# Performance work log

Hardware: AMD Instinct MI355X
Metric: run time of the kernel (lower is better)

The kernel has to match this reference:

```python
import jax, jax.numpy as jnp
import numpy as np

B = 8192
I = 1024
H = 1024


def setup_inputs() -> dict:
    key = jax.random.key(0)
    ks = jax.random.split(key, 7)
    s_in = 1.0 / np.sqrt(I)
    s_h = 1.0 / np.sqrt(H)
    return {
        "x_current": jax.random.normal(ks[0], (B, I), dtype=jnp.float32),
        "c_previous": jax.random.normal(ks[1], (B, H), dtype=jnp.float32),
        "h_previous": jax.random.normal(ks[2], (B, H), dtype=jnp.float32),
        # stacked gate weights, order (i, f, o, g); equivalent to 8 small nn.Linear
        "Wx": jax.random.normal(ks[3], (4 * H, I), dtype=jnp.float32) * s_in,
        "bx": jax.random.normal(ks[4], (4 * H,), dtype=jnp.float32) * s_in,
        "Wh": jax.random.normal(ks[5], (4 * H, H), dtype=jnp.float32) * s_h,
        "bh": jax.random.normal(ks[6], (4 * H,), dtype=jnp.float32) * s_h,
    }


def reference(x_current, c_previous, h_previous, Wx, bx, Wh, bh):
    # two fused GEMMs covering all 8 original linears: [B, 4H]
    gates = (jnp.einsum("bi,gi->bg", x_current, Wx) + bx
             + jnp.einsum("bh,gh->bg", h_previous, Wh) + bh)
    i_g, f_g, o_g, g_g = jnp.split(gates, 4, axis=-1)
    input_gate = jax.nn.sigmoid(i_g)
    forget_gate = jax.nn.sigmoid(f_g)
    output_gate = jax.nn.sigmoid(o_g)
    g_current = jnp.tanh(g_g)
    c_current = forget_gate * c_previous + input_gate * g_current
    h_current = output_gate * jnp.tanh(c_current)
    return (c_current, h_current)
```

## Files before the change

### kernel.cpp

```cpp
#include <hip/hip_runtime.h>
#include <hip/hip_bf16.h>

#define Bsz 8192
#define Isz 1024
#define Hsz 1024
#define Ksz 2048
#define Nsz 4096

#define BM 128
#define BN 128
#define BK 64

typedef __attribute__((ext_vector_type(8))) short bf16x8;
typedef __attribute__((ext_vector_type(4))) float f32x4;
typedef __attribute__((ext_vector_type(8))) unsigned short ushort8;

__device__ __forceinline__ void async_copy16(const void* g, void* l) {
  __builtin_amdgcn_global_load_lds(
      (const __attribute__((address_space(1))) void*)g,
      (__attribute__((address_space(3))) void*)l, 16, 0, 0);
}

__device__ __forceinline__ float sigmoid_f(float x) {
  return 1.0f / (1.0f + __expf(-x));
}
__device__ __forceinline__ float tanh_f(float x) {
  x = fminf(15.0f, fmaxf(-15.0f, x));
  const float e = __expf(-2.0f * x);
  return (1.0f - e) / (1.0f + e);
}

__device__ __forceinline__ unsigned short bfc(float f) {
  return __builtin_bit_cast(unsigned short, __float2bfloat16(f));
}
__device__ __forceinline__ ushort8 cvt8v(float4 v0, float4 v1) {
  ushort8 o;
  o[0] = bfc(v0.x); o[1] = bfc(v0.y); o[2] = bfc(v0.z); o[3] = bfc(v0.w);
  o[4] = bfc(v1.x); o[5] = bfc(v1.y); o[6] = bfc(v1.z); o[7] = bfc(v1.w);
  return o;
}

__global__ __launch_bounds__(256) void prep_kernel(
    const float* __restrict__ x, const float* __restrict__ h,
    const float* __restrict__ Wx, const float* __restrict__ Wh,
    const float* __restrict__ bx, const float* __restrict__ bh,
    __hip_bfloat16* __restrict__ Abf, __hip_bfloat16* __restrict__ Wbf,
    float* __restrict__ bsum) {
  const int idx = blockIdx.x * 256 + threadIdx.x;
  const int ATH = (Bsz * Ksz) / 8;
  if (idx < ATH) {
    const int b = idx >> 8;
    const int k = (idx & 255) << 3;
    const float* src = (k < Isz) ? (x + (size_t)b * Isz + k)
                                 : (h + (size_t)b * Hsz + (k - Isz));
    const float4 v0 = ((const float4*)src)[0];
    const float4 v1 = ((const float4*)src)[1];
    *(ushort8*)(Abf + (size_t)b * Ksz + k) = cvt8v(v0, v1);
  } else {
    const int t2 = idx - ATH;
    const int r = t2 >> 8;
    const int k = (t2 & 255) << 3;
    const int hh = r >> 2, g = r & 3;
    const float* src = (k < Isz) ? (Wx + (size_t)(g * Hsz + hh) * Isz + k)
                                 : (Wh + (size_t)(g * Hsz + hh) * Hsz + (k - Isz));
    const float4 v0 = ((const float4*)src)[0];
    const float4 v1 = ((const float4*)src)[1];
    *(ushort8*)(Wbf + (size_t)r * Ksz + k) = cvt8v(v0, v1);
  }
  if (idx < Nsz) {
    const int hh = idx >> 2, g = idx & 3;
    bsum[idx] = bx[g * Hsz + hh] + bh[g * Hsz + hh];
  }
}

__global__ __launch_bounds__(256) void lstm_gemm_kernel(
    const __hip_bfloat16* __restrict__ A,
    const __hip_bfloat16* __restrict__ W,
    const float* __restrict__ bsum,
    const float* __restrict__ c_prev,
    float* __restrict__ c_out,
    float* __restrict__ h_out) {
  __shared__ ulong2 smem_raw[2048];
  __hip_bfloat16* As = (__hip_bfloat16*)smem_raw;
  __hip_bfloat16* Bs = As + BM * BK;

  const int tid = threadIdx.x;
  const int lane = tid & 63;
  const int wave = tid >> 6;
  const int wm = wave & 1;
  const int wn = wave >> 1;
  const int row0 = blockIdx.x * BM;
  const int col0 = blockIdx.y * BN;

  const __hip_bfloat16* Ag = A + (size_t)row0 * Ksz;
  const __hip_bfloat16* Wg = W + (size_t)col0 * Ksz;

  int srow[4], sofs[4];
#pragma unroll
  for (int p = 0; p < 4; p++) {
    const int c = tid + p * 256;
    srow[p] = c >> 3;
    sofs[p] = ((c & 7) ^ ((c >> 3) & 7)) << 3;
  }

  f32x4 acc[4][4] = {};

  const int q = lane >> 4;
  const int cl = lane & 15;
  const int phi = cl & 7;

  for (int kt = 0; kt < Ksz; kt += BK) {
    __syncthreads();
#pragma unroll
    for (int p = 0; p < 4; p++)
      async_copy16(Ag + (size_t)srow[p] * Ksz + kt + sofs[p],
                   (char*)As + (tid + p * 256) * 16);
#pragma unroll
    for (int p = 0; p < 4; p++)
      async_copy16(Wg + (size_t)srow[p] * Ksz + kt + sofs[p],
                   (char*)Bs + (tid + p * 256) * 16);
    __syncthreads();

#pragma unroll
    for (int ks = 0; ks < 2; ks++) {
      const int jsw = ((ks * 4 + q) ^ phi) << 3;
      bf16x8 af[4], bfr[4];
#pragma unroll
      for (int i = 0; i < 4; i++)
        af[i] = *(const bf16x8*)(As + (wm * 64 + i * 16 + cl) * BK + jsw);
#pragma unroll
      for (int j = 0; j < 4; j++)
        bfr[j] = *(const bf16x8*)(Bs + (wn * 64 + j * 16 + cl) * BK + jsw);
#pragma unroll
      for (int i = 0; i < 4; i++)
#pragma unroll
        for (int j = 0; j < 4; j++)
          acc[i][j] = __builtin_amdgcn_mfma_f32_16x16x32_bf16(
              af[i], bfr[j], acc[i][j], 0, 0, 0);
    }
  }

  __syncthreads();
  float* E = (float*)smem_raw + wave * (16 * 68);

  float bj[4];
#pragma unroll
  for (int j = 0; j < 4; j++)
    bj[j] = bsum[col0 + wn * 64 + j * 16 + cl];

  const int hw = (col0 >> 2) + wn * 16;
  const int r16 = lane >> 2;
  const int tt = lane & 3;

#pragma unroll
  for (int i = 0; i < 4; i++) {
#pragma unroll
    for (int j = 0; j < 4; j++)
#pragma unroll
      for (int r = 0; r < 4; r++)
        E[(q * 4 + r) * 68 + j * 16 + cl] = acc[i][j][r] + bj[j];
    __builtin_amdgcn_wave_barrier();
    const float* Er = E + r16 * 68 + tt * 16;
    const float4 f0 = ((const float4*)Er)[0];
    const float4 f1 = ((const float4*)Er)[1];
    const float4 f2 = ((const float4*)Er)[2];
    const float4 f3 = ((const float4*)Er)[3];

    const int row = row0 + wm * 64 + i * 16 + r16;
    const size_t off = (size_t)row * Hsz + hw + tt * 4;
    const float4 cp4 = *(const float4*)(c_prev + off);
    float4 c4, h4;
    {
      const float cn = sigmoid_f(f0.y) * cp4.x + sigmoid_f(f0.x) * tanh_f(f0.w);
      c4.x = cn; h4.x = sigmoid_f(f0.z) * tanh_f(cn);
    }
    {
      const float cn = sigmoid_f(f1.y) * cp4.y + sigmoid_f(f1.x) * tanh_f(f1.w);
      c4.y = cn; h4.y = sigmoid_f(f1.z) * tanh_f(cn);
    }
    {
      const float cn = sigmoid_f(f2.y) * cp4.z + sigmoid_f(f2.x) * tanh_f(f2.w);
      c4.z = cn; h4.z = sigmoid_f(f2.z) * tanh_f(cn);
    }
    {
      const float cn = sigmoid_f(f3.y) * cp4.w + sigmoid_f(f3.x) * tanh_f(f3.w);
      c4.w = cn; h4.w = sigmoid_f(f3.z) * tanh_f(cn);
    }
    *(float4*)(c_out + off) = c4;
    *(float4*)(h_out + off) = h4;
    __builtin_amdgcn_wave_barrier();
  }
}

extern "C" void kernel_launch(void* const* d_in, const int* in_sizes, int n_in,
                              void* d_out, int out_size, void* d_ws,
                              size_t ws_size, hipStream_t stream) {
  (void)in_sizes; (void)n_in; (void)out_size; (void)ws_size;
  const float* x  = (const float*)d_in[0];
  const float* cp = (const float*)d_in[1];
  const float* hp = (const float*)d_in[2];
  const float* Wx = (const float*)d_in[3];
  const float* bx = (const float*)d_in[4];
  const float* Wh = (const float*)d_in[5];
  const float* bh = (const float*)d_in[6];

  __hip_bfloat16* Abf = (__hip_bfloat16*)d_ws;
  __hip_bfloat16* Wbf = Abf + (size_t)Bsz * Ksz;
  float* bsum = (float*)(Wbf + (size_t)Nsz * Ksz);

  float* c_out = (float*)d_out;
  float* h_out = c_out + (size_t)Bsz * Hsz;

  const int total_threads = (Bsz * Ksz) / 8 + (Nsz * Ksz) / 8;
  prep_kernel<<<total_threads / 256, 256, 0, stream>>>(x, hp, Wx, Wh, bx, bh,
                                                       Abf, Wbf, bsum);
  dim3 grid(Bsz / BM, Nsz / BN);
  lstm_gemm_kernel<<<grid, 256, 0, stream>>>(Abf, Wbf, bsum, cp, c_out, h_out);
}
```

Measured before the change: 341.3 us.

## Enlarge GEMM tile to 256x256 with double-buffered async LDS pipeline

Raises the block tile from 128x128 to 256x256 with 512 threads (8 waves, 2x4), and double-buffers the A and B tiles in LDS. Global-to-LDS async copies for the next K-steps are spread across four compute phases and interleaved with MFMAs under explicit vmcnt waits and barriers. It also remaps the 1D grid with a swizzle for better L2 reuse. The aim is to hide load latency behind MFMA work and cut global traffic per FLOP, at the cost of 128KB of LDS, more registers and more barriers.

```diff
diff --git a/kernel.cpp b/kernel.cpp
--- a/kernel.cpp
+++ b/kernel.cpp
@@ -7,9 +7,10 @@
 #define Ksz 2048
 #define Nsz 4096
 
-#define BM 128
-#define BN 128
+#define BM 256
+#define BN 256
 #define BK 64
+#define NT (Ksz / BK)
 
 typedef __attribute__((ext_vector_type(8))) short bf16x8;
 typedef __attribute__((ext_vector_type(4))) float f32x4;
@@ -73,92 +74,148 @@
   }
 }
 
-__global__ __launch_bounds__(256) void lstm_gemm_kernel(
+__global__ __launch_bounds__(512, 2) void lstm_gemm_kernel(
     const __hip_bfloat16* __restrict__ A,
     const __hip_bfloat16* __restrict__ W,
     const float* __restrict__ bsum,
     const float* __restrict__ c_prev,
     float* __restrict__ c_out,
     float* __restrict__ h_out) {
-  __shared__ ulong2 smem_raw[2048];
-  __hip_bfloat16* As = (__hip_bfloat16*)smem_raw;
-  __hip_bfloat16* Bs = As + BM * BK;
+  __shared__ ulong2 smem_raw[8192];
+  __hip_bfloat16* const As = (__hip_bfloat16*)smem_raw;
+  __hip_bfloat16* const Bs = As + 2 * BM * BK;
+  char* const smemc = (char*)smem_raw;
 
   const int tid = threadIdx.x;
   const int lane = tid & 63;
   const int wave = tid >> 6;
-  const int wm = wave & 1;
-  const int wn = wave >> 1;
-  const int row0 = blockIdx.x * BM;
-  const int col0 = blockIdx.y * BN;
-
-  const __hip_bfloat16* Ag = A + (size_t)row0 * Ksz;
-  const __hip_bfloat16* Wg = W + (size_t)col0 * Ksz;
-
-  int srow[4], sofs[4];
-#pragma unroll
-  for (int p = 0; p < 4; p++) {
-    const int c = tid + p * 256;
-    srow[p] = c >> 3;
-    sofs[p] = ((c & 7) ^ ((c >> 3) & 7)) << 3;
-  }
-
-  f32x4 acc[4][4] = {};
+  const int wm = wave >> 2;
+  const int wn = wave & 3;
+
+  const int orig = blockIdx.x;
+  const int swz = (orig & 7) * 64 + (orig >> 3);
+  const int bx = swz & 31;
+  const int by = swz >> 5;
+  const int row0 = bx * BM;
+  const int col0 = by * BN;
+
+  const __hip_bfloat16* const Ag = A + (size_t)row0 * Ksz;
+  const __hip_bfloat16* const Wg = W + (size_t)col0 * Ksz;
+
+  const int sr = tid >> 3;
+  const int so = ((tid & 7) ^ (sr & 7)) << 3;
+
+  auto stage = [&](const __hip_bfloat16* gsrc ,
+                   char* lhalf ) {
+#pragma unroll
+    for (int p = 0; p < 2; ++p)
+      async_copy16(gsrc + (size_t)(sr + p * 64) * Ksz,
+                   lhalf + (tid + p * 512) * 16);
+  };
 
   const int q = lane >> 4;
   const int cl = lane & 15;
   const int phi = cl & 7;
-
-  for (int kt = 0; kt < Ksz; kt += BK) {
-    __syncthreads();
-#pragma unroll
-    for (int p = 0; p < 4; p++)
-      async_copy16(Ag + (size_t)srow[p] * Ksz + kt + sofs[p],
-                   (char*)As + (tid + p * 256) * 16);
-#pragma unroll
-    for (int p = 0; p < 4; p++)
-      async_copy16(Wg + (size_t)srow[p] * Ksz + kt + sofs[p],
-                   (char*)Bs + (tid + p * 256) * 16);
-    __syncthreads();
-
-#pragma unroll
-    for (int ks = 0; ks < 2; ks++) {
-      const int jsw = ((ks * 4 + q) ^ phi) << 3;
-      bf16x8 af[4], bfr[4];
-#pragma unroll
-      for (int i = 0; i < 4; i++)
-        af[i] = *(const bf16x8*)(As + (wm * 64 + i * 16 + cl) * BK + jsw);
-#pragma unroll
-      for (int j = 0; j < 4; j++)
-        bfr[j] = *(const bf16x8*)(Bs + (wn * 64 + j * 16 + cl) * BK + jsw);
-#pragma unroll
-      for (int i = 0; i < 4; i++)
-#pragma unroll
-        for (int j = 0; j < 4; j++)
-          acc[i][j] = __builtin_amdgcn_mfma_f32_16x16x32_bf16(
-              af[i], bfr[j], acc[i][j], 0, 0, 0);
+  const int swz0 = ((0 + q) ^ phi) << 3;
+  const int swz1 = ((4 + q) ^ phi) << 3;
+  const int aoff0 = (wm * 128 + cl) * BK + swz0;
+  const int aoff1 = (wm * 128 + cl) * BK + swz1;
+  const int boff0 = (wn * 64 + cl) * BK + swz0;
+  const int boff1 = (wn * 64 + cl) * BK + swz1;
+
+  stage(Ag + so, smemc);
+  stage(Ag + (size_t)128 * Ksz + so, smemc + 16384);
+  stage(Wg + so, smemc + 65536);
+  stage(Wg + (size_t)128 * Ksz + so, smemc + 65536 + 16384);
+  __builtin_amdgcn_sched_barrier(0);
+  stage(Wg + BK + so, smemc + 65536 + 32768);
+  stage(Wg + BK + (size_t)128 * Ksz + so, smemc + 65536 + 32768 + 16384);
+  asm volatile("s_waitcnt vmcnt(4)" ::: "memory");
+  __builtin_amdgcn_sched_barrier(0);
+  __builtin_amdgcn_s_barrier();
+  asm volatile("" ::: "memory");
+  __builtin_amdgcn_sched_barrier(0);
+
+  f32x4 acc[8][4] = {};
+
+  for (int t = 0; t < NT; ++t) {
+    const __hip_bfloat16* const Asb = As + (t & 1) * (BM * BK);
+    const __hip_bfloat16* const Bsb = Bs + (t & 1) * (BM * BK);
+    char* const nA = smemc + (((t + 1) & 1) * 32768);
+    char* const nB = smemc + 65536 + ((t & 1) * 32768);
+    const int kA = (t + 1) * BK;
+    const int kB = (t + 2) * BK;
+    const bool doA = (t + 1) < NT;
+    const bool doB = (t + 2) < NT;
+
+    bf16x8 bfr[4][2];
+
+#pragma unroll
+    for (int ph = 0; ph < 4; ++ph) {
+      const int m0 = 2 * ph;
+      bf16x8 a00 = *(const bf16x8*)(Asb + aoff0 + m0 * (16 * BK));
+      bf16x8 a01 = *(const bf16x8*)(Asb + aoff1 + m0 * (16 * BK));
+      bf16x8 a10 = *(const bf16x8*)(Asb + aoff0 + (m0 + 1) * (16 * BK));
+      bf16x8 a11 = *(const bf16x8*)(Asb + aoff1 + (m0 + 1) * (16 * BK));
+      if (ph == 0) {
+#pragma unroll
+        for (int n = 0; n < 4; ++n) {
+          bfr[n][0] = *(const bf16x8*)(Bsb + boff0 + n * (16 * BK));
+          bfr[n][1] = *(const bf16x8*)(Bsb + boff1 + n * (16 * BK));
+        }
+      }
+      if (ph == 0 && doA) stage(Ag + kA + so, nA);
+      if (ph == 1 && doA) stage(Ag + kA + (size_t)128 * Ksz + so, nA + 16384);
+      if (ph == 2 && doB) stage(Wg + kB + so, nB);
+      if (ph == 3 && doB) stage(Wg + kB + (size_t)128 * Ksz + so, nB + 16384);
+
+      __builtin_amdgcn_sched_barrier(0);
+      __builtin_amdgcn_s_barrier();
+      asm volatile("" ::: "memory");
+      __builtin_amdgcn_sched_barrier(0);
+
+      __builtin_amdgcn_s_setprio(1);
+#pragma unroll
+      for (int n = 0; n < 4; ++n) {
+        acc[m0][n]     = __builtin_amdgcn_mfma_f32_16x16x32_bf16(a00, bfr[n][0], acc[m0][n], 0, 0, 0);
+        acc[m0][n]     = __builtin_amdgcn_mfma_f32_16x16x32_bf16(a01, bfr[n][1], acc[m0][n], 0, 0, 0);
+        acc[m0 + 1][n] = __builtin_amdgcn_mfma_f32_16x16x32_bf16(a10, bfr[n][0], acc[m0 + 1][n], 0, 0, 0);
+        acc[m0 + 1][n] = __builtin_amdgcn_mfma_f32_16x16x32_bf16(a11, bfr[n][1], acc[m0 + 1][n], 0, 0, 0);
+      }
+      __builtin_amdgcn_s_setprio(0);
+      __builtin_amdgcn_sched_barrier(0);
+      if (ph == 3) {
+        if (t < NT - 2) {
+          asm volatile("s_waitcnt vmcnt(4)" ::: "memory");
+        } else if (t == NT - 2) {
+          asm volatile("s_waitcnt vmcnt(0)" ::: "memory");
+        }
+      }
+      __builtin_amdgcn_s_barrier();
+      asm volatile("" ::: "memory");
+      __builtin_amdgcn_sched_barrier(0);
     }
   }
 
   __syncthreads();
-  float* E = (float*)smem_raw + wave * (16 * 68);
+  float* const E = (float*)smem_raw + wave * (16 * 68);
 
   float bj[4];
 #pragma unroll
-  for (int j = 0; j < 4; j++)
-    bj[j] = bsum[col0 + wn * 64 + j * 16 + cl];
+  for (int n = 0; n < 4; ++n)
+    bj[n] = bsum[col0 + wn * 64 + n * 16 + cl];
 
   const int hw = (col0 >> 2) + wn * 16;
   const int r16 = lane >> 2;
   const int tt = lane & 3;
 
 #pragma unroll
-  for (int i = 0; i < 4; i++) {
-#pragma unroll
-    for (int j = 0; j < 4; j++)
-#pragma unroll
-      for (int r = 0; r < 4; r++)
-        E[(q * 4 + r) * 68 + j * 16 + cl] = acc[i][j][r] + bj[j];
+  for (int i = 0; i < 8; ++i) {
+#pragma unroll
+    for (int n = 0; n < 4; ++n)
+#pragma unroll
+      for (int r = 0; r < 4; ++r)
+        E[(q * 4 + r) * 68 + n * 16 + cl] = acc[i][n][r] + bj[n];
     __builtin_amdgcn_wave_barrier();
     const float* Er = E + r16 * 68 + tt * 16;
     const float4 f0 = ((const float4*)Er)[0];
@@ -166,7 +223,7 @@
     const float4 f2 = ((const float4*)Er)[2];
     const float4 f3 = ((const float4*)Er)[3];
 
-    const int row = row0 + wm * 64 + i * 16 + r16;
+    const int row = row0 + wm * 128 + i * 16 + r16;
     const size_t off = (size_t)row * Hsz + hw + tt * 4;
     const float4 cp4 = *(const float4*)(c_prev + off);
     float4 c4, h4;
@@ -214,6 +271,6 @@
   const int total_threads = (Bsz * Ksz) / 8 + (Nsz * Ksz) / 8;
   prep_kernel<<<total_threads / 256, 256, 0, stream>>>(x, hp, Wx, Wh, bx, bh,
                                                        Abf, Wbf, bsum);
-  dim3 grid(Bsz / BM, Nsz / BN);
-  lstm_gemm_kernel<<<grid, 256, 0, stream>>>(Abf, Wbf, bsum, cp, c_out, h_out);
-}
+  dim3 grid(Bsz / BM * (Nsz / BN));
+  lstm_gemm_kernel<<<grid, 512, 0, stream>>>(Abf, Wbf, bsum, cp, c_out, h_out);
+}
```

Measured after the change: 310.3 us. -9.1%, faster.
